# Performance work log

Hardware: AMD Instinct MI355X
Metric: run time of the kernel (lower is better)

Reference implementation:

```python
import jax, jax.numpy as jnp
import numpy as np

GN_GROUPS = 32
GN_EPS = 1e-5


def conv3x3(x, w, b=None):
    # x: [B,C,H,W], w: [O,I,3,3]
    y = jax.lax.conv_general_dilated(x, w, (1, 1), 'SAME',
                                     dimension_numbers=('NCHW', 'OIHW', 'NCHW'))
    if b is not None:
        y = y + b[None, :, None, None]
    return y


def group_norm(x, gamma, beta):
    B, C, H, W = x.shape
    xg = x.reshape(B, GN_GROUPS, C // GN_GROUPS, H, W)
    mu = xg.mean(axis=(2, 3, 4), keepdims=True)
    var = ((xg - mu) ** 2).mean(axis=(2, 3, 4), keepdims=True)
    xn = ((xg - mu) * jax.lax.rsqrt(var + GN_EPS)).reshape(B, C, H, W)
    return xn * gamma[None, :, None, None] + beta[None, :, None, None]


def tower(x, ws, gammas, betas):
    # ws: [n_conv, C, C, 3, 3]; conv(bias=False) -> GroupNorm -> ReLU, n_conv times
    for i in range(ws.shape[0]):
        x = jax.nn.relu(group_norm(conv3x3(x, ws[i]), gammas[i], betas[i]))
    return x


def setup_inputs() -> dict:
    key = jax.random.key(0)
    ks = jax.random.split(key, 20)
    C, n_conv, n_fg = 256, 4, 20  # n_class - 1 = 20
    prior = 0.01
    B = 2
    sizes = [(100, 100), (50, 50), (25, 25), (13, 13), (7, 7)]
    inp = {}
    for i, (h, w) in enumerate(sizes):
        inp[f'feat{i}'] = jax.random.normal(ks[i], (B, C, h, w), dtype=jnp.float32)
    std = 0.01  # init_conv_std
    inp['cls_tw_w'] = std * jax.random.normal(ks[5], (n_conv, C, C, 3, 3), dtype=jnp.float32)
    inp['cls_tw_g'] = jnp.ones((n_conv, C), dtype=jnp.float32)
    inp['cls_tw_b'] = jnp.zeros((n_conv, C), dtype=jnp.float32)
    inp['box_tw_w'] = std * jax.random.normal(ks[6], (n_conv, C, C, 3, 3), dtype=jnp.float32)
    inp['box_tw_g'] = jnp.ones((n_conv, C), dtype=jnp.float32)
    inp['box_tw_b'] = jnp.zeros((n_conv, C), dtype=jnp.float32)
    inp['cls_pred_w'] = std * jax.random.normal(ks[7], (n_fg, C, 3, 3), dtype=jnp.float32)
    prior_bias = -np.log((1.0 - prior) / prior)
    inp['cls_pred_b'] = jnp.full((n_fg,), prior_bias, dtype=jnp.float32)
    inp['box_pred_w'] = std * jax.random.normal(ks[8], (4, C, 3, 3), dtype=jnp.float32)
    inp['box_pred_b'] = jnp.zeros((4,), dtype=jnp.float32)
    inp['ctr_pred_w'] = std * jax.random.normal(ks[9], (1, C, 3, 3), dtype=jnp.float32)
    inp['ctr_pred_b'] = jnp.zeros((1,), dtype=jnp.float32)
    inp['scales'] = jnp.ones((5,), dtype=jnp.float32)
    return inp


def reference(feat0, feat1, feat2, feat3, feat4,
              cls_tw_w, cls_tw_g, cls_tw_b,
              box_tw_w, box_tw_g, box_tw_b,
              cls_pred_w, cls_pred_b,
              box_pred_w, box_pred_b,
              ctr_pred_w, ctr_pred_b,
              scales):
    feats = [feat0, feat1, feat2, feat3, feat4]
    logits, bboxes, centers = [], [], []
    for i, feat in enumerate(feats):
        c = tower(feat, cls_tw_w, cls_tw_g, cls_tw_b)
        logits.append(conv3x3(c, cls_pred_w, cls_pred_b))
        centers.append(conv3x3(c, ctr_pred_w, ctr_pred_b))
        b = tower(feat, box_tw_w, box_tw_g, box_tw_b)
        bboxes.append(jnp.exp(conv3x3(b, box_pred_w, box_pred_b) * scales[i]))
    return tuple(logits + bboxes + centers)
```

## Files before the change

### kernel.cpp

```cpp
#include <hip/hip_runtime.h>
#include <hip/hip_bf16.h>
#include <cstdint>

typedef unsigned short u16;
typedef __attribute__((ext_vector_type(8))) short short8;
typedef __attribute__((ext_vector_type(4))) float floatx4;

#define PA_TOTAL 13696
#define CCH 256
#define KTOT 2304

struct Tables {
  int H[5], W[5], P[5], base[5], tile0[5];
  int lb[5], bb[5], cb[5];
};
struct FeatPtrs { const float* f[5]; };
struct ConvArgs {
  const u16* X[2];
  const u16* Wt[2];
  const u16* zbuf;
  u16* outB[2];
  float* stats;
  float* dout;
  const float* biasCls; const float* biasCtr; const float* biasBox; const float* scales;
};

__device__ __forceinline__ u16 f2bf(float f) {
  union { float f; unsigned u; } v; v.f = f;
  unsigned r = v.u + 0x7fffu + ((v.u >> 16) & 1u);
  return (u16)(r >> 16);
}
__device__ __forceinline__ float bf2f(u16 h) {
  union { unsigned u; float f; } v; v.u = ((unsigned)h) << 16;
  return v.f;
}

__device__ __forceinline__ void gl2lds16(const u16* g, u16* l) {
  __builtin_amdgcn_global_load_lds((const __attribute__((address_space(1))) unsigned int*)g,
                                   (__attribute__((address_space(3))) unsigned int*)l, 16, 0, 0);
}

__global__ void reorder_w(const float* __restrict__ w, u16* __restrict__ out, int n) {
  int idx = blockIdx.x * 256 + threadIdx.x;
  if (idx >= n) return;
  int k = idx % KTOT;
  int row = idx / KTOT;
  int tap = k >> 8, ic = k & 255;
  out[idx] = f2bf(w[(size_t)row * KTOT + ic * 9 + tap]);
}

__global__ void reorder_pred_cls(const float* __restrict__ cls_w, const float* __restrict__ ctr_w,
                                 u16* __restrict__ out) {
  int idx = blockIdx.x * 256 + threadIdx.x;
  int k = idx % KTOT;
  int row = idx / KTOT;
  int tap = k >> 8, ic = k & 255;
  float v = (row < 20) ? cls_w[(size_t)row * KTOT + ic * 9 + tap] : ctr_w[ic * 9 + tap];
  out[idx] = f2bf(v);
}

__global__ void convert_inputs(FeatPtrs fp, u16* __restrict__ out, Tables tb) {
  __shared__ float tile[32][33];
  const int pt = blockIdx.x, c32 = blockIdx.y, b = blockIdx.z;
  const int p0 = pt * 32;
  int lvl = 0;
#pragma unroll
  for (int i = 1; i < 5; ++i) if (p0 >= tb.base[i]) lvl = i;
  const int P = tb.P[lvl];
  const int pl0 = p0 - tb.base[lvl];
  const int r = threadIdx.x >> 5, col = threadIdx.x & 31;
  const float* src = fp.f[lvl] + ((size_t)b * CCH + c32 * 32) * P;
#pragma unroll
  for (int i = 0; i < 4; ++i) {
    int crow = r + i * 8;
    int pl = pl0 + col;
    tile[crow][col] = (pl < P) ? src[(size_t)crow * P + pl] : 0.f;
  }
  __syncthreads();
#pragma unroll
  for (int i = 0; i < 4; ++i) {
    int px = r + i * 8;
    out[((size_t)b * PA_TOTAL + p0 + px) * CCH + c32 * 32 + col] = f2bf(tile[col][px]);
  }
}

template <int MODE>
__global__ __launch_bounds__(256) void conv_mfma(ConvArgs a, Tables tb) {
  const int L = blockIdx.x + (MODE == 0 ? 107 : 108) * (blockIdx.y + 2 * blockIdx.z);
  const int xcd = L & 7, slot = L >> 3;
  int tower, mt, b, t;
  if (MODE == 0) {
    tower = xcd >> 2; mt = (xcd >> 1) & 1; b = xcd & 1; t = slot;
  } else {
    tower = xcd >> 2; mt = 0; b = (xcd >> 1) & 1; t = slot * 2 + (xcd & 1);
    if (t >= 107) return;
  }
  int lvl = 0;
#pragma unroll
  for (int i = 1; i < 5; ++i) if (t >= tb.tile0[i]) lvl = i;
  const int H = tb.H[lvl], W = tb.W[lvl], P = tb.P[lvl], base = tb.base[lvl];
  const int n0 = (t - tb.tile0[lvl]) * 128;

  const int tid = threadIdx.x;
  const int lane = tid & 63, wv = tid >> 6;
  const int wm = wv >> 1, wn = wv & 1;

  __shared__ u16 ldsX[128 * 64];
  __shared__ u16 ldsW[128 * 64];

  const u16* X = a.X[tower];
  const u16* Wt = a.Wt[tower];
  const u16* zbuf = a.zbuf;

  const int qsw = (((lane & 7) ^ (lane >> 3))) * 8;
  int prow[4];
  unsigned mask9[4];
  const u16* wsrc[4];
  u16 *ldsXd[4], *ldsWd[4];
#pragma unroll
  for (int t4 = 0; t4 < 4; ++t4) {
    int row = (t4 * 4 + wv) * 8 + (lane >> 3);
    prow[t4] = n0 + row;
    int rr = prow[t4] / W, cc = prow[t4] - rr * W;
    unsigned m = 0;
#pragma unroll
    for (int tap = 0; tap < 9; ++tap) {
      const int dh = tap / 3 - 1, dw = tap % 3 - 1;
      bool v = ((unsigned)(rr + dh) < (unsigned)H) & ((unsigned)(cc + dw) < (unsigned)W);
      m |= ((unsigned)v) << tap;
    }
    mask9[t4] = m;
    wsrc[t4] = Wt + (size_t)(mt * 128 + row) * KTOT + qsw;
    ldsXd[t4] = ldsX + (t4 * 4 + wv) * 512;
    ldsWd[t4] = ldsW + (t4 * 4 + wv) * 512;
  }
  const u16* Xbp = X + ((size_t)b * PA_TOTAL + base) * CCH;

  const int arow = lane & 15, rsw = lane & 7, kq0 = lane >> 4;
  int aoff[2][4], boff[2][4];
#pragma unroll
  for (int h = 0; h < 2; ++h) {
    int csw = (((h * 4 + kq0) ^ rsw)) * 8;
#pragma unroll
    for (int i = 0; i < 4; ++i) {
      aoff[h][i] = (wm * 64 + i * 16 + arow) * 64 + csw;
      boff[h][i] = (wn * 64 + i * 16 + arow) * 64 + csw;
    }
  }

  floatx4 acc[4][4];
#pragma unroll
  for (int i = 0; i < 4; ++i)
#pragma unroll
    for (int j = 0; j < 4; ++j) acc[i][j] = (floatx4)0.f;

#pragma unroll 1
  for (int icb = 0; icb < 4; ++icb) {
#pragma unroll
    for (int tap = 0; tap < 9; ++tap) {
      const int dh = tap / 3 - 1, dw = tap % 3 - 1;
      const int dpos = dh * W + dw;
      const int ko = tap * 256 + icb * 64;
      __syncthreads();
#pragma unroll
      for (int t4 = 0; t4 < 4; ++t4) {
        const u16* src = ((mask9[t4] >> tap) & 1)
            ? (Xbp + (size_t)(prow[t4] + dpos) * CCH + qsw + icb * 64) : zbuf;
        gl2lds16(src, ldsXd[t4]);
      }
#pragma unroll
      for (int t4 = 0; t4 < 4; ++t4) gl2lds16(wsrc[t4] + ko, ldsWd[t4]);
      __syncthreads();
#pragma unroll
      for (int h = 0; h < 2; ++h) {
        short8 af[4], bv[4];
#pragma unroll
        for (int i = 0; i < 4; ++i) af[i] = *(const short8*)(ldsW + aoff[h][i]);
#pragma unroll
        for (int j = 0; j < 4; ++j) bv[j] = *(const short8*)(ldsX + boff[h][j]);
#pragma unroll
        for (int i = 0; i < 4; ++i)
#pragma unroll
          for (int j = 0; j < 4; ++j)
            acc[i][j] = __builtin_amdgcn_mfma_f32_16x16x32_bf16(af[i], bv[j], acc[i][j], 0, 0, 0);
      }
    }
  }

  const int quad = lane >> 4, col = lane & 15;
  if (MODE == 0) {
    u16* convB = a.outB[tower];
    float s[4] = {0.f, 0.f, 0.f, 0.f}, ss[4] = {0.f, 0.f, 0.f, 0.f};
#pragma unroll
    for (int j = 0; j < 4; ++j) {
      int pl = n0 + wn * 64 + j * 16 + col;
      bool valid = pl < P;
      u16* dst = convB + ((size_t)b * PA_TOTAL + base + pl) * CCH + mt * 128 + wm * 64 + quad * 4;
#pragma unroll
      for (int i = 0; i < 4; ++i) {
        ushort4 hv;
#pragma unroll
        for (int r = 0; r < 4; ++r) {
          u16 hh = f2bf(acc[i][j][r]);
          ((u16*)&hv)[r] = hh;
          float vr = bf2f(hh);
          if (valid) { s[i] += vr; ss[i] += vr * vr; }
        }
        if (valid) *(ushort4*)(dst + i * 16) = hv;
      }
    }
#pragma unroll
    for (int i = 0; i < 4; ++i) {
#pragma unroll
      for (int off = 16; off >= 1; off >>= 1) {
        s[i] += __shfl_down(s[i], off, 64);
        ss[i] += __shfl_down(ss[i], off, 64);
      }
    }
    if ((lane & 31) == 0) {
      int half = lane >> 5;
#pragma unroll
      for (int i = 0; i < 4; ++i) {
        float* st = a.stats + tower * 640 +
                    ((size_t)((b * 5 + lvl) * 32 + mt * 16 + wm * 8 + i * 2 + half)) * 2;
        atomicAdd(st, s[i]);
        atomicAdd(st + 1, ss[i]);
      }
    }
  } else {
    float* dout = a.dout;
    if (tower == 0) {
#pragma unroll
      for (int j = 0; j < 4; ++j) {
        int pl = n0 + wn * 64 + j * 16 + col;
        if (pl >= P) continue;
#pragma unroll
        for (int i = 0; i < 4; ++i) {
          int ocb = wm * 64 + i * 16 + quad * 4;
#pragma unroll
          for (int r = 0; r < 4; ++r) {
            int oc = ocb + r;
            float v = acc[i][j][r];
            if (oc < 20)       dout[tb.lb[lvl] + ((size_t)b * 20 + oc) * P + pl] = v + a.biasCls[oc];
            else if (oc == 20) dout[tb.cb[lvl] + (size_t)b * P + pl] = v + a.biasCtr[0];
          }
        }
      }
    } else {
      float sc = a.scales[lvl];
#pragma unroll
      for (int j = 0; j < 4; ++j) {
        int pl = n0 + wn * 64 + j * 16 + col;
        if (pl >= P) continue;
#pragma unroll
        for (int i = 0; i < 4; ++i) {
          int ocb = wm * 64 + i * 16 + quad * 4;
#pragma unroll
          for (int r = 0; r < 4; ++r) {
            int oc = ocb + r;
            if (oc < 4)
              dout[tb.bb[lvl] + ((size_t)b * 4 + oc) * P + pl] = expf((acc[i][j][r] + a.biasBox[oc]) * sc);
          }
        }
      }
    }
  }
}

__global__ void gn_norm(const u16* __restrict__ c0, const u16* __restrict__ c1,
                        const float* __restrict__ stats,
                        const float* __restrict__ g0, const float* __restrict__ b0,
                        const float* __restrict__ g1, const float* __restrict__ b1,
                        u16* __restrict__ a0, u16* __restrict__ a1, Tables tb) {
  const int tower = blockIdx.y;
  const u16* convB = tower ? c1 : c0;
  const float* gamma = tower ? g1 : g0;
  const float* beta = tower ? b1 : b0;
  u16* act = tower ? a1 : a0;
  int idx = blockIdx.x * 256 + threadIdx.x;
  int c8 = idx & 31;
  int rest = idx >> 5;
  int p = rest % PA_TOTAL;
  int b = rest / PA_TOTAL;
  int lvl = 0;
#pragma unroll
  for (int i = 1; i < 5; ++i) if (p >= tb.base[i]) lvl = i;
  if (p - tb.base[lvl] >= tb.P[lvl]) return;
  const float* st = stats + tower * 640 + ((size_t)((b * 5 + lvl) * 32 + c8)) * 2;
  float cnt = 8.f * (float)tb.P[lvl];
  float mean = st[0] / cnt;
  float var = st[1] / cnt - mean * mean;
  float inv = rsqrtf(var + 1e-5f);
  const short8 x = *(const short8*)(convB + ((size_t)b * PA_TOTAL + p) * CCH + c8 * 8);
  short8 o;
#pragma unroll
  for (int j = 0; j < 8; ++j) {
    float v = bf2f((u16)x[j]);
    float y = (v - mean) * inv * gamma[c8 * 8 + j] + beta[c8 * 8 + j];
    y = fmaxf(y, 0.f);
    o[j] = (short)f2bf(y);
  }
  *(short8*)(act + ((size_t)b * PA_TOTAL + p) * CCH + c8 * 8) = o;
}

extern "C" void kernel_launch(void* const* d_in, const int* in_sizes, int n_in,
                              void* d_out, int out_size, void* d_ws, size_t ws_size,
                              hipStream_t stream) {
  const float* feat[5];
  for (int i = 0; i < 5; ++i) feat[i] = (const float*)d_in[i];
  const float* cls_tw_w  = (const float*)d_in[5];
  const float* cls_tw_g  = (const float*)d_in[6];
  const float* cls_tw_b  = (const float*)d_in[7];
  const float* box_tw_w  = (const float*)d_in[8];
  const float* box_tw_g  = (const float*)d_in[9];
  const float* box_tw_b  = (const float*)d_in[10];
  const float* cls_pred_w = (const float*)d_in[11];
  const float* cls_pred_b = (const float*)d_in[12];
  const float* box_pred_w = (const float*)d_in[13];
  const float* box_pred_b = (const float*)d_in[14];
  const float* ctr_pred_w = (const float*)d_in[15];
  const float* ctr_pred_b = (const float*)d_in[16];
  const float* scales     = (const float*)d_in[17];
  float* out = (float*)d_out;

  char* ws = (char*)d_ws;
  u16*   zbuf   = (u16*)(ws);
  float* stats  = (float*)(ws + 512);
  u16*   WrCls  = (u16*)(ws + 8192);
  u16*   WrBox  = (u16*)(ws + 8192 + 4718592);
  u16*   WrPCls = (u16*)(ws + 8192 + 2 * 4718592);
  u16*   WrPBox = (u16*)(ws + 8192 + 2 * 4718592 + 589824);
  u16*   bufIn   = (u16*)(ws + 10625024);
  u16*   bufAct0 = (u16*)(ws + 10625024 + 1 * (size_t)14024704);
  u16*   bufAct1 = (u16*)(ws + 10625024 + 2 * (size_t)14024704);
  u16*   bufCv0  = (u16*)(ws + 10625024 + 3 * (size_t)14024704);
  u16*   bufCv1  = (u16*)(ws + 10625024 + 4 * (size_t)14024704);

  Tables tb = { {100,50,25,13,7}, {100,50,25,13,7}, {10000,2500,625,169,49},
                {0,10112,12672,13312,13568}, {0,79,99,104,106},
                {0,400000,500000,525000,531760},
                {533720,613720,633720,638720,640072},
                {640464,660464,665464,666714,667052} };

  hipMemsetAsync(zbuf, 0, 512, stream);
  hipMemsetAsync(WrPCls, 0, 589824, stream);
  hipMemsetAsync(WrPBox, 0, 589824, stream);

  reorder_w<<<9216, 256, 0, stream>>>(cls_tw_w, WrCls, 1024 * KTOT);
  reorder_w<<<9216, 256, 0, stream>>>(box_tw_w, WrBox, 1024 * KTOT);
  reorder_pred_cls<<<189, 256, 0, stream>>>(cls_pred_w, ctr_pred_w, WrPCls);
  reorder_w<<<36, 256, 0, stream>>>(box_pred_w, WrPBox, 4 * KTOT);

  FeatPtrs fp = {{feat[0], feat[1], feat[2], feat[3], feat[4]}};
  convert_inputs<<<dim3(PA_TOTAL / 32, 8, 2), 256, 0, stream>>>(fp, bufIn, tb);

  ConvArgs a;
  a.zbuf = zbuf; a.stats = stats; a.dout = out;
  a.biasCls = cls_pred_b; a.biasCtr = ctr_pred_b; a.biasBox = box_pred_b; a.scales = scales;
  a.outB[0] = bufCv0; a.outB[1] = bufCv1;

  for (int s = 0; s < 4; ++s) {
    a.X[0] = (s == 0) ? bufIn : bufAct0;
    a.X[1] = (s == 0) ? bufIn : bufAct1;
    a.Wt[0] = WrCls + (size_t)s * 256 * KTOT;
    a.Wt[1] = WrBox + (size_t)s * 256 * KTOT;
    hipMemsetAsync(stats, 0, 5120, stream);
    conv_mfma<0><<<dim3(107, 2, 4), 256, 0, stream>>>(a, tb);
    gn_norm<<<dim3(3424, 2), 256, 0, stream>>>(bufCv0, bufCv1, stats,
                                               cls_tw_g + s * 256, cls_tw_b + s * 256,
                                               box_tw_g + s * 256, box_tw_b + s * 256,
                                               bufAct0, bufAct1, tb);
  }
  a.X[0] = bufAct0; a.X[1] = bufAct1;
  a.Wt[0] = WrPCls; a.Wt[1] = WrPBox;
  conv_mfma<1><<<dim3(108, 2, 2), 256, 0, stream>>>(a, tb);
}
```

Measured before the change: 670.4 us.

## Double-buffer LDS tiles to overlap global loads with MFMA compute

Doubles the LDS buffers for the activation and weight tiles and prefetches the next (tap, channel-block) tile into the alternate buffer while MFMAs run on the current one. A prologue loads the first tile, and one barrier per iteration replaces the previous two. The aim is to hide global-to-LDS latency behind matrix math. The cost is twice the shared memory per block, which may reduce how many blocks fit on a CU.

```diff
diff --git a/kernel.cpp b/kernel.cpp
--- a/kernel.cpp
+++ b/kernel.cpp
@@ -105,8 +105,8 @@
   const int lane = tid & 63, wv = tid >> 6;
   const int wm = wv >> 1, wn = wv & 1;
 
-  __shared__ u16 ldsX[128 * 64];
-  __shared__ u16 ldsW[128 * 64];
+  __shared__ u16 ldsX[2 * 128 * 64];
+  __shared__ u16 ldsW[2 * 128 * 64];
 
   const u16* X = a.X[tower];
   const u16* Wt = a.Wt[tower];
@@ -116,7 +116,7 @@
   int prow[4];
   unsigned mask9[4];
   const u16* wsrc[4];
-  u16 *ldsXd[4], *ldsWd[4];
+  int ldso[4];
 #pragma unroll
   for (int t4 = 0; t4 < 4; ++t4) {
     int row = (t4 * 4 + wv) * 8 + (lane >> 3);
@@ -131,8 +131,7 @@
     }
     mask9[t4] = m;
     wsrc[t4] = Wt + (size_t)(mt * 128 + row) * KTOT + qsw;
-    ldsXd[t4] = ldsX + (t4 * 4 + wv) * 512;
-    ldsWd[t4] = ldsW + (t4 * 4 + wv) * 512;
+    ldso[t4] = (t4 * 4 + wv) * 512;
   }
   const u16* Xbp = X + ((size_t)b * PA_TOTAL + base) * CCH;
 
@@ -154,30 +153,50 @@
 #pragma unroll
     for (int j = 0; j < 4; ++j) acc[i][j] = (floatx4)0.f;
 
+  {
+    const int dpos0 = -W - 1;
+#pragma unroll
+    for (int t4 = 0; t4 < 4; ++t4) {
+      const u16* src = (mask9[t4] & 1)
+          ? (Xbp + (size_t)(prow[t4] + dpos0) * CCH + qsw) : zbuf;
+      gl2lds16(src, ldsX + ldso[t4]);
+    }
+#pragma unroll
+    for (int t4 = 0; t4 < 4; ++t4) gl2lds16(wsrc[t4], ldsW + ldso[t4]);
+  }
+
 #pragma unroll 1
   for (int icb = 0; icb < 4; ++icb) {
+    const int cb = icb & 1;
 #pragma unroll
     for (int tap = 0; tap < 9; ++tap) {
-      const int dh = tap / 3 - 1, dw = tap % 3 - 1;
-      const int dpos = dh * W + dw;
-      const int ko = tap * 256 + icb * 64;
+      const int cur = cb ^ (tap & 1);
       __syncthreads();
-#pragma unroll
-      for (int t4 = 0; t4 < 4; ++t4) {
-        const u16* src = ((mask9[t4] >> tap) & 1)
-            ? (Xbp + (size_t)(prow[t4] + dpos) * CCH + qsw + icb * 64) : zbuf;
-        gl2lds16(src, ldsXd[t4]);
-      }
-#pragma unroll
-      for (int t4 = 0; t4 < 4; ++t4) gl2lds16(wsrc[t4] + ko, ldsWd[t4]);
-      __syncthreads();
+      if (!(icb == 3 && tap == 8)) {
+        const int ntap = (tap == 8) ? 0 : tap + 1;
+        const int nicb = (tap == 8) ? icb + 1 : icb;
+        const int ndh = ntap / 3;
+        const int ndpos = (ndh - 1) * W + (ntap - 3 * ndh - 1);
+        const int nko = ntap * 256 + nicb * 64;
+        u16* lx = ldsX + (1 - cur) * 8192;
+        u16* lw = ldsW + (1 - cur) * 8192;
+#pragma unroll
+        for (int t4 = 0; t4 < 4; ++t4) {
+          const u16* src = ((mask9[t4] >> ntap) & 1)
+              ? (Xbp + (size_t)(prow[t4] + ndpos) * CCH + qsw + nicb * 64) : zbuf;
+          gl2lds16(src, lx + ldso[t4]);
+        }
+#pragma unroll
+        for (int t4 = 0; t4 < 4; ++t4) gl2lds16(wsrc[t4] + nko, lw + ldso[t4]);
+      }
+      const int co = cur * 8192;
 #pragma unroll
       for (int h = 0; h < 2; ++h) {
         short8 af[4], bv[4];
 #pragma unroll
-        for (int i = 0; i < 4; ++i) af[i] = *(const short8*)(ldsW + aoff[h][i]);
-#pragma unroll
-        for (int j = 0; j < 4; ++j) bv[j] = *(const short8*)(ldsX + boff[h][j]);
+        for (int i = 0; i < 4; ++i) af[i] = *(const short8*)(ldsW + co + aoff[h][i]);
+#pragma unroll
+        for (int j = 0; j < 4; ++j) bv[j] = *(const short8*)(ldsX + co + boff[h][j]);
 #pragma unroll
         for (int i = 0; i < 4; ++i)
 #pragma unroll
```

Measured after the change: 952.6 us. 42.1% more time.

## Shrink prediction-head conv to 32 output rows and coalesce weight reorder via LDS

Applied to the files above, without the earlier changes.

The prediction-head conv (MODE 1) previously computed a full 128-row output tile even though only 21 or 4 output channels are used. It now loads and multiplies only 32 weight rows (16 per wave row) with a single accumulator row, which cuts MFMA work and weight traffic for the final conv. Weight reordering now stages each row in shared memory so global reads are coalesced instead of strided by 9. The risk is that the 16-row-per-wave mapping for prediction outputs must stay consistent with the zero-padded weight layout.

```diff
diff --git a/kernel.cpp b/kernel.cpp
--- a/kernel.cpp
+++ b/kernel.cpp
@@ -40,23 +40,35 @@
                                    (__attribute__((address_space(3))) unsigned int*)l, 16, 0, 0);
 }
 
-__global__ void reorder_w(const float* __restrict__ w, u16* __restrict__ out, int n) {
-  int idx = blockIdx.x * 256 + threadIdx.x;
-  if (idx >= n) return;
-  int k = idx % KTOT;
-  int row = idx / KTOT;
-  int tap = k >> 8, ic = k & 255;
-  out[idx] = f2bf(w[(size_t)row * KTOT + ic * 9 + tap]);
+__global__ void reorder_rows(const float* __restrict__ src, u16* __restrict__ out) {
+  __shared__ float row[KTOT];
+  const int r = blockIdx.x;
+  const float* s = src + (size_t)r * KTOT;
+  u16* o = out + (size_t)r * KTOT;
+#pragma unroll
+  for (int j = 0; j < 9; ++j) row[threadIdx.x + j * 256] = s[threadIdx.x + j * 256];
+  __syncthreads();
+#pragma unroll
+  for (int j = 0; j < 9; ++j) {
+    int k = threadIdx.x + j * 256;
+    o[k] = f2bf(row[(k & 255) * 9 + (k >> 8)]);
+  }
 }
 
 __global__ void reorder_pred_cls(const float* __restrict__ cls_w, const float* __restrict__ ctr_w,
                                  u16* __restrict__ out) {
-  int idx = blockIdx.x * 256 + threadIdx.x;
-  int k = idx % KTOT;
-  int row = idx / KTOT;
-  int tap = k >> 8, ic = k & 255;
-  float v = (row < 20) ? cls_w[(size_t)row * KTOT + ic * 9 + tap] : ctr_w[ic * 9 + tap];
-  out[idx] = f2bf(v);
+  __shared__ float row[KTOT];
+  const int r = blockIdx.x;
+  const float* s = (r < 20) ? (cls_w + (size_t)r * KTOT) : ctr_w;
+  u16* o = out + (size_t)r * KTOT;
+#pragma unroll
+  for (int j = 0; j < 9; ++j) row[threadIdx.x + j * 256] = s[threadIdx.x + j * 256];
+  __syncthreads();
+#pragma unroll
+  for (int j = 0; j < 9; ++j) {
+    int k = threadIdx.x + j * 256;
+    o[k] = f2bf(row[(k & 255) * 9 + (k >> 8)]);
+  }
 }
 
 __global__ void convert_inputs(FeatPtrs fp, u16* __restrict__ out, Tables tb) {
@@ -86,6 +98,7 @@
 
 template <int MODE>
 __global__ __launch_bounds__(256) void conv_mfma(ConvArgs a, Tables tb) {
+  constexpr int NI = (MODE == 0) ? 4 : 1;
   const int L = blockIdx.x + (MODE == 0 ? 107 : 108) * (blockIdx.y + 2 * blockIdx.z);
   const int xcd = L & 7, slot = L >> 3;
   int tower, mt, b, t;
@@ -106,7 +119,7 @@
   const int wm = wv >> 1, wn = wv & 1;
 
   __shared__ u16 ldsX[128 * 64];
-  __shared__ u16 ldsW[128 * 64];
+  __shared__ u16 ldsW[(MODE == 0 ? 128 : 32) * 64];
 
   const u16* X = a.X[tower];
   const u16* Wt = a.Wt[tower];
@@ -115,8 +128,7 @@
   const int qsw = (((lane & 7) ^ (lane >> 3))) * 8;
   int prow[4];
   unsigned mask9[4];
-  const u16* wsrc[4];
-  u16 *ldsXd[4], *ldsWd[4];
+  int ldso[4];
 #pragma unroll
   for (int t4 = 0; t4 < 4; ++t4) {
     int row = (t4 * 4 + wv) * 8 + (lane >> 3);
@@ -130,9 +142,13 @@
       m |= ((unsigned)v) << tap;
     }
     mask9[t4] = m;
-    wsrc[t4] = Wt + (size_t)(mt * 128 + row) * KTOT + qsw;
-    ldsXd[t4] = ldsX + (t4 * 4 + wv) * 512;
-    ldsWd[t4] = ldsW + (t4 * 4 + wv) * 512;
+    ldso[t4] = (t4 * 4 + wv) * 512;
+  }
+  const u16* wsrc[4];
+#pragma unroll
+  for (int t4 = 0; t4 < NI; ++t4) {
+    int wrow = (MODE == 0) ? ((t4 * 4 + wv) * 8 + (lane >> 3)) : (wv * 8 + (lane >> 3));
+    wsrc[t4] = Wt + (size_t)(mt * 128 + wrow) * KTOT + qsw;
   }
   const u16* Xbp = X + ((size_t)b * PA_TOTAL + base) * CCH;
 
@@ -142,15 +158,17 @@
   for (int h = 0; h < 2; ++h) {
     int csw = (((h * 4 + kq0) ^ rsw)) * 8;
 #pragma unroll
-    for (int i = 0; i < 4; ++i) {
-      aoff[h][i] = (wm * 64 + i * 16 + arow) * 64 + csw;
-      boff[h][i] = (wn * 64 + i * 16 + arow) * 64 + csw;
-    }
-  }
-
-  floatx4 acc[4][4];
-#pragma unroll
-  for (int i = 0; i < 4; ++i)
+    for (int i = 0; i < NI; ++i) {
+      int rowb = (MODE == 0) ? (wm * 64 + i * 16) : (wm * 16);
+      aoff[h][i] = (rowb + arow) * 64 + csw;
+    }
+#pragma unroll
+    for (int i = 0; i < 4; ++i) boff[h][i] = (wn * 64 + i * 16 + arow) * 64 + csw;
+  }
+
+  floatx4 acc[NI][4];
+#pragma unroll
+  for (int i = 0; i < NI; ++i)
 #pragma unroll
     for (int j = 0; j < 4; ++j) acc[i][j] = (floatx4)0.f;
 
@@ -166,20 +184,21 @@
       for (int t4 = 0; t4 < 4; ++t4) {
         const u16* src = ((mask9[t4] >> tap) & 1)
             ? (Xbp + (size_t)(prow[t4] + dpos) * CCH + qsw + icb * 64) : zbuf;
-        gl2lds16(src, ldsXd[t4]);
-      }
-#pragma unroll
-      for (int t4 = 0; t4 < 4; ++t4) gl2lds16(wsrc[t4] + ko, ldsWd[t4]);
+        gl2lds16(src, ldsX + ldso[t4]);
+      }
+#pragma unroll
+      for (int t4 = 0; t4 < NI; ++t4)
+        gl2lds16(wsrc[t4] + ko, ldsW + (MODE == 0 ? ldso[t4] : wv * 512));
       __syncthreads();
 #pragma unroll
       for (int h = 0; h < 2; ++h) {
-        short8 af[4], bv[4];
-#pragma unroll
-        for (int i = 0; i < 4; ++i) af[i] = *(const short8*)(ldsW + aoff[h][i]);
+        short8 af[NI], bv[4];
+#pragma unroll
+        for (int i = 0; i < NI; ++i) af[i] = *(const short8*)(ldsW + aoff[h][i]);
 #pragma unroll
         for (int j = 0; j < 4; ++j) bv[j] = *(const short8*)(ldsX + boff[h][j]);
 #pragma unroll
-        for (int i = 0; i < 4; ++i)
+        for (int i = 0; i < NI; ++i)
 #pragma unroll
           for (int j = 0; j < 4; ++j)
             acc[i][j] = __builtin_amdgcn_mfma_f32_16x16x32_bf16(af[i], bv[j], acc[i][j], 0, 0, 0);
@@ -234,16 +253,13 @@
       for (int j = 0; j < 4; ++j) {
         int pl = n0 + wn * 64 + j * 16 + col;
         if (pl >= P) continue;
-#pragma unroll
-        for (int i = 0; i < 4; ++i) {
-          int ocb = wm * 64 + i * 16 + quad * 4;
-#pragma unroll
-          for (int r = 0; r < 4; ++r) {
-            int oc = ocb + r;
-            float v = acc[i][j][r];
-            if (oc < 20)       dout[tb.lb[lvl] + ((size_t)b * 20 + oc) * P + pl] = v + a.biasCls[oc];
-            else if (oc == 20) dout[tb.cb[lvl] + (size_t)b * P + pl] = v + a.biasCtr[0];
-          }
+        int ocb = wm * 16 + quad * 4;
+#pragma unroll
+        for (int r = 0; r < 4; ++r) {
+          int oc = ocb + r;
+          float v = acc[0][j][r];
+          if (oc < 20)       dout[tb.lb[lvl] + ((size_t)b * 20 + oc) * P + pl] = v + a.biasCls[oc];
+          else if (oc == 20) dout[tb.cb[lvl] + (size_t)b * P + pl] = v + a.biasCtr[0];
         }
       }
     } else {
@@ -252,15 +268,12 @@
       for (int j = 0; j < 4; ++j) {
         int pl = n0 + wn * 64 + j * 16 + col;
         if (pl >= P) continue;
-#pragma unroll
-        for (int i = 0; i < 4; ++i) {
-          int ocb = wm * 64 + i * 16 + quad * 4;
-#pragma unroll
-          for (int r = 0; r < 4; ++r) {
-            int oc = ocb + r;
-            if (oc < 4)
-              dout[tb.bb[lvl] + ((size_t)b * 4 + oc) * P + pl] = expf((acc[i][j][r] + a.biasBox[oc]) * sc);
-          }
+        int ocb = wm * 16 + quad * 4;
+#pragma unroll
+        for (int r = 0; r < 4; ++r) {
+          int oc = ocb + r;
+          if (oc < 4)
+            dout[tb.bb[lvl] + ((size_t)b * 4 + oc) * P + pl] = expf((acc[0][j][r] + a.biasBox[oc]) * sc);
         }
       }
     }
@@ -346,10 +359,10 @@
   hipMemsetAsync(WrPCls, 0, 589824, stream);
   hipMemsetAsync(WrPBox, 0, 589824, stream);
 
-  reorder_w<<<9216, 256, 0, stream>>>(cls_tw_w, WrCls, 1024 * KTOT);
-  reorder_w<<<9216, 256, 0, stream>>>(box_tw_w, WrBox, 1024 * KTOT);
-  reorder_pred_cls<<<189, 256, 0, stream>>>(cls_pred_w, ctr_pred_w, WrPCls);
-  reorder_w<<<36, 256, 0, stream>>>(box_pred_w, WrPBox, 4 * KTOT);
+  reorder_rows<<<1024, 256, 0, stream>>>(cls_tw_w, WrCls);
+  reorder_rows<<<1024, 256, 0, stream>>>(box_tw_w, WrBox);
+  reorder_pred_cls<<<21, 256, 0, stream>>>(cls_pred_w, ctr_pred_w, WrPCls);
+  reorder_rows<<<4, 256, 0, stream>>>(box_pred_w, WrPBox);
 
   FeatPtrs fp = {{feat[0], feat[1], feat[2], feat[3], feat[4]}};
   convert_inputs<<<dim3(PA_TOTAL / 32, 8, 2), 256, 0, stream>>>(fp, bufIn, tb);
```

After: 645.3 us. 1.04x faster.
